# Optimization experiments

Hardware: AMD Instinct MI355X
Metric: run time of the kernel (lower is better)

## Reference

```python
import jax, jax.numpy as jnp
import numpy as np

NUM_HEADS = 12


def _qkv_split(x, qkv_w, num_heads):
    B, N, C = x.shape
    hd = C // num_heads
    qkv = (x @ qkv_w).reshape(B, N, 3, num_heads, hd)
    qkv = jnp.transpose(qkv, (2, 0, 3, 1, 4))  # [3, B, H, N, hd]
    return qkv[0], qkv[1], qkv[2]


def setup_inputs() -> dict:
    key = jax.random.key(0)
    k1, k2, k3, k4 = jax.random.split(key, 4)
    B, N, C = 8, 1024, 768
    s = 0.02
    return {
        "x1": jax.random.normal(k1, (B, N, C), dtype=jnp.float32),
        "x2": jax.random.normal(k2, (B, N, C), dtype=jnp.float32),
        "qkv_w": jax.random.normal(k3, (C, 3 * C), dtype=jnp.float32) * s,
        "proj_w": jax.random.normal(k4, (C, C), dtype=jnp.float32) * s,
        "proj_b": jnp.zeros((C,), dtype=jnp.float32),
    }


def reference(x1, x2, qkv_w, proj_w, proj_b):
    B, N, C = x1.shape
    H = NUM_HEADS
    hd = C // H
    scale = hd ** (-0.5)

    q, k, v = _qkv_split(x1, qkv_w, H)    # each [B, H, N, hd]
    q2, k2, v2 = _qkv_split(x2, qkv_w, H)

    # self-attention branch: q attends to k/v (from x1)
    attn1 = jax.nn.softmax(jnp.einsum('bhqd,bhkd->bhqk', q, k) * scale, axis=-1)
    o1 = jnp.einsum('bhqk,bhkd->bhqd', attn1, v)

    # cross-attention branch: same q attends to k2/v2 (from x2)
    attn2 = jax.nn.softmax(jnp.einsum('bhqd,bhkd->bhqk', q, k2) * scale, axis=-1)
    o2 = jnp.einsum('bhqk,bhkd->bhqd', attn2, v2)

    o1 = jnp.transpose(o1, (0, 2, 1, 3)).reshape(B, N, C) @ proj_w + proj_b
    o2 = jnp.transpose(o2, (0, 2, 1, 3)).reshape(B, N, C) @ proj_w + proj_b
    return (o1, o2)
```

## Files before the change

kernel.cpp:

```cpp
#include <hip/hip_runtime.h>
#include <hip/hip_bf16.h>

#define N_ 1024
#define C_ 768
#define H_ 12

typedef unsigned short u16;
typedef __attribute__((ext_vector_type(8))) short bf16x8;
typedef __attribute__((ext_vector_type(4))) float f32x4;
typedef __attribute__((ext_vector_type(16))) float f32x16;

#define MFMA16(a, b, c) __builtin_amdgcn_mfma_f32_16x16x32_bf16(a, b, c, 0, 0, 0)
#define MFMA32(a, b, c) __builtin_amdgcn_mfma_f32_32x32x16_bf16(a, b, c, 0, 0, 0)

#define GLDS16(gp, lp) __builtin_amdgcn_global_load_lds(                     \
    (const __attribute__((address_space(1))) void*)(gp),                     \
    (__attribute__((address_space(3))) void*)(lp), 16, 0, 0)

__device__ __forceinline__ u16 f2bu(float x) {
    unsigned u = __float_as_uint(x);
    unsigned r = (u + 0x7fffu + ((u >> 16) & 1u)) >> 16;
    return (u16)r;
}

__device__ __forceinline__ unsigned cvtpk(float a, float b) {
    unsigned d;
    asm("v_cvt_pk_bf16_f32 %0, %1, %2" : "=v"(d) : "v"(a), "v"(b));
    return d;
}

__global__ __launch_bounds__(256) void cvt_x(
    const float* __restrict__ x1, const float* __restrict__ x2,
    u16* __restrict__ d1, u16* __restrict__ d2)
{
    const size_t G = 786432;
    for (size_t i = (size_t)blockIdx.x * 256 + threadIdx.x; i < 2 * G;
         i += (size_t)gridDim.x * 256) {
        const float* src = (i < G) ? x1 : x2;
        u16* dst = (i < G) ? d1 : d2;
        size_t g = (i < G) ? i : i - G;
        float4 f0 = ((const float4*)src)[g * 2];
        float4 f1 = ((const float4*)src)[g * 2 + 1];
        ushort4 lo, hi;
        lo.x = f2bu(f0.x); lo.y = f2bu(f0.y); lo.z = f2bu(f0.z); lo.w = f2bu(f0.w);
        hi.x = f2bu(f1.x); hi.y = f2bu(f1.y); hi.z = f2bu(f1.z); hi.w = f2bu(f1.w);
        ((ushort4*)dst)[g * 2] = lo;
        ((ushort4*)dst)[g * 2 + 1] = hi;
    }
}

__global__ __launch_bounds__(256) void tr_cvt(
    const float* __restrict__ W, u16* __restrict__ WT, int R, int CC)
{
    __shared__ float t[32][33];
    const int tx = threadIdx.x & 31, ty = threadIdx.x >> 5;
    const int c0 = blockIdx.x * 32, r0 = blockIdx.y * 32;
#pragma unroll
    for (int i = 0; i < 4; ++i) {
        int r = ty + i * 8;
        t[r][tx] = W[(size_t)(r0 + r) * CC + c0 + tx];
    }
    __syncthreads();
#pragma unroll
    for (int i = 0; i < 4; ++i) {
        int c = ty + i * 8;
        WT[(size_t)(c0 + c) * R + r0 + tx] = f2bu(t[tx][c]);
    }
}

__global__ __launch_bounds__(256) void qkv_gemm(
    const u16* __restrict__ A1, const u16* __restrict__ A2,
    const u16* __restrict__ BT, u16* __restrict__ qd,
    u16* __restrict__ k1d, u16* __restrict__ k2d,
    u16* __restrict__ vt1d, u16* __restrict__ vt2d)
{
    __shared__ u16 As[2][128 * 64];
    __shared__ u16 Bs[2][128 * 64];
    const int tid = threadIdx.x;
    const int w = tid >> 6, lane = tid & 63;
    const int c31 = lane & 31, h = lane >> 5;
    const int wm = w >> 1, wn = w & 1;
    const int id = blockIdx.x;
    const int xcd = id & 7, j = id >> 3;
    const int by = xcd * 8 + j / 30;
    const int bx = j % 30;
    const bool first = bx < 18;
    const u16* A = first ? A1 : A2;
    const int row0 = by * 128;
    const int nc0 = first ? bx * 128 : 768 + (bx - 18) * 128;

    f32x16 acc[2][2];
#pragma unroll
    for (int i = 0; i < 2; ++i)
#pragma unroll
        for (int jj = 0; jj < 2; ++jj)
#pragma unroll
            for (int e = 0; e < 16; ++e) acc[i][jj][e] = 0.f;

    int aoff[4], boff[4];
    {
        const int srow = tid >> 3;
        const int sch = ((tid & 7) ^ (srow & 7)) * 8;
#pragma unroll
        for (int i = 0; i < 4; ++i) {
            int row = i * 32 + srow;
            aoff[i] = (row0 + row) * C_ + sch;
            boff[i] = (nc0 + row) * C_ + sch;
        }
    }
    char* adst0 = (char*)&As[0][0] + w * 1024;
    char* bdst0 = (char*)&Bs[0][0] + w * 1024;
    auto stage = [&](int buf, int k0) {
#pragma unroll
        for (int i = 0; i < 4; ++i) {
            GLDS16(A + aoff[i] + k0, adst0 + buf * 16384 + i * 4096);
            GLDS16(BT + boff[i] + k0, bdst0 + buf * 16384 + i * 4096);
        }
    };

    const int ra0 = wm * 64 + c31, ra1 = ra0 + 32;
    const int rb0 = wn * 64 + c31, rb1 = rb0 + 32;

    stage(0, 0);
    for (int kt = 0; kt < 12; ++kt) {
        const int buf = kt & 1;
        if (kt < 11) {
            stage(buf ^ 1, (kt + 1) * 64);
            asm volatile("s_waitcnt vmcnt(8)" ::: "memory");
        } else {
            asm volatile("s_waitcnt vmcnt(0)" ::: "memory");
        }
        __builtin_amdgcn_s_barrier();
        const char* abase = (const char*)&As[0][0] + buf * 16384;
        const char* bbase = (const char*)&Bs[0][0] + buf * 16384;
#pragma unroll
        for (int kh = 0; kh < 4; ++kh) {
            bf16x8 a0 = *(const bf16x8*)(abase + ra0 * 128 + (((2 * kh + h) ^ (ra0 & 7)) * 16));
            bf16x8 a1 = *(const bf16x8*)(abase + ra1 * 128 + (((2 * kh + h) ^ (ra1 & 7)) * 16));
            bf16x8 b0 = *(const bf16x8*)(bbase + rb0 * 128 + (((2 * kh + h) ^ (rb0 & 7)) * 16));
            bf16x8 b1 = *(const bf16x8*)(bbase + rb1 * 128 + (((2 * kh + h) ^ (rb1 & 7)) * 16));
            acc[0][0] = MFMA32(a0, b0, acc[0][0]);
            acc[0][1] = MFMA32(a0, b1, acc[0][1]);
            acc[1][0] = MFMA32(a1, b0, acc[1][0]);
            acc[1][1] = MFMA32(a1, b1, acc[1][1]);
        }
        asm volatile("" ::: "memory");
        __builtin_amdgcn_s_barrier();
    }

    u16* kd  = first ? k1d : k2d;
    u16* vtd = first ? vt1d : vt2d;
    const int abscol = nc0 + wn * 64;
    const int sec = abscol / C_;
    const int hh = (abscol % C_) >> 6;
    const float scl = (sec == 0) ? 0.180336877f : 1.0f;
#pragma unroll
    for (int mt = 0; mt < 2; ++mt)
#pragma unroll
        for (int nt = 0; nt < 2; ++nt)
#pragma unroll
            for (int r = 0; r < 16; ++r) {
                int row = row0 + wm * 64 + mt * 32 + (r & 3) + 8 * (r >> 2) + 4 * h;
                int b = row >> 10, n = row & 1023;
                int d = nt * 32 + c31;
                u16 val = f2bu(acc[mt][nt][r] * scl);
                size_t bh = (size_t)(b * H_ + hh);
                if (sec == 0)      qd[(bh * N_ + n) * 64 + d] = val;
                else if (sec == 1) kd[(bh * N_ + n) * 64 + d] = val;
                else {
                    int nprm = (n & ~63) | (((n & 15) << 2) | ((n >> 4) & 3));
                    vtd[(bh * 64 + d) * N_ + nprm] = val;
                }
            }
}

__global__ __launch_bounds__(256) void proj_gemm(
    const u16* __restrict__ A1, const u16* __restrict__ A2,
    const u16* __restrict__ BT, const float* __restrict__ bias,
    float* __restrict__ out)
{
    __shared__ u16 As[2][128 * 64];
    __shared__ u16 Bs[2][128 * 64];
    const int tid = threadIdx.x;
    const int w = tid >> 6, lane = tid & 63;
    const int c31 = lane & 31, h = lane >> 5;
    const int wm = w >> 1, wn = w & 1;
    const int sel = blockIdx.y >> 6;
    const u16* A = sel ? A2 : A1;
    float* op = out + (size_t)sel * 8192 * C_;
    const int row0 = (blockIdx.y & 63) * 128;
    const int nc0 = blockIdx.x * 128;

    f32x16 acc[2][2];
#pragma unroll
    for (int i = 0; i < 2; ++i)
#pragma unroll
        for (int jj = 0; jj < 2; ++jj)
#pragma unroll
            for (int e = 0; e < 16; ++e) acc[i][jj][e] = 0.f;

    int aoff[4], boff[4];
    {
        const int srow = tid >> 3;
        const int sch = ((tid & 7) ^ (srow & 7)) * 8;
#pragma unroll
        for (int i = 0; i < 4; ++i) {
            int row = i * 32 + srow;
            aoff[i] = (row0 + row) * C_ + sch;
            boff[i] = (nc0 + row) * C_ + sch;
        }
    }
    char* adst0 = (char*)&As[0][0] + w * 1024;
    char* bdst0 = (char*)&Bs[0][0] + w * 1024;
    auto stage = [&](int buf, int k0) {
#pragma unroll
        for (int i = 0; i < 4; ++i) {
            GLDS16(A + aoff[i] + k0, adst0 + buf * 16384 + i * 4096);
            GLDS16(BT + boff[i] + k0, bdst0 + buf * 16384 + i * 4096);
        }
    };

    const int ra0 = wm * 64 + c31, ra1 = ra0 + 32;
    const int rb0 = wn * 64 + c31, rb1 = rb0 + 32;

    stage(0, 0);
    for (int kt = 0; kt < 12; ++kt) {
        const int buf = kt & 1;
        if (kt < 11) {
            stage(buf ^ 1, (kt + 1) * 64);
            asm volatile("s_waitcnt vmcnt(8)" ::: "memory");
        } else {
            asm volatile("s_waitcnt vmcnt(0)" ::: "memory");
        }
        __builtin_amdgcn_s_barrier();
        const char* abase = (const char*)&As[0][0] + buf * 16384;
        const char* bbase = (const char*)&Bs[0][0] + buf * 16384;
#pragma unroll
        for (int kh = 0; kh < 4; ++kh) {
            bf16x8 a0 = *(const bf16x8*)(abase + ra0 * 128 + (((2 * kh + h) ^ (ra0 & 7)) * 16));
            bf16x8 a1 = *(const bf16x8*)(abase + ra1 * 128 + (((2 * kh + h) ^ (ra1 & 7)) * 16));
            bf16x8 b0 = *(const bf16x8*)(bbase + rb0 * 128 + (((2 * kh + h) ^ (rb0 & 7)) * 16));
            bf16x8 b1 = *(const bf16x8*)(bbase + rb1 * 128 + (((2 * kh + h) ^ (rb1 & 7)) * 16));
            acc[0][0] = MFMA32(a0, b0, acc[0][0]);
            acc[0][1] = MFMA32(a0, b1, acc[0][1]);
            acc[1][0] = MFMA32(a1, b0, acc[1][0]);
            acc[1][1] = MFMA32(a1, b1, acc[1][1]);
        }
        asm volatile("" ::: "memory");
        __builtin_amdgcn_s_barrier();
    }

#pragma unroll
    for (int mt = 0; mt < 2; ++mt)
#pragma unroll
        for (int nt = 0; nt < 2; ++nt)
#pragma unroll
            for (int r = 0; r < 16; ++r) {
                int row = row0 + wm * 64 + mt * 32 + (r & 3) + 8 * (r >> 2) + 4 * h;
                int col = nc0 + wn * 64 + nt * 32 + c31;
                op[(size_t)row * C_ + col] = acc[mt][nt][r] + bias[col];
            }
}

__global__ __launch_bounds__(256) void attn_mfma(
    const u16* __restrict__ Q,
    const u16* __restrict__ K1, const u16* __restrict__ VT1,
    const u16* __restrict__ K2, const u16* __restrict__ VT2,
    u16* __restrict__ O1, u16* __restrict__ O2)
{
    __shared__ u16 Ks[2][64 * 64];
    __shared__ u16 Vs[2][64 * 64];
    __shared__ u16 Ps[4][32 * 72];
    const int tid = threadIdx.x;
    const int w = tid >> 6, lane = tid & 63;
    const int g = lane >> 4, ln = lane & 15;
    const int id = blockIdx.x;
    const int xcd = id & 7, j = id >> 3;
    const int unit = j >> 3;
    const int qb = j & 7;
    const int br = unit >= 12;
    const int bh = xcd * 12 + (br ? unit - 12 : unit);
    const int qw = qb * 128 + w * 32;
    const size_t hb = (size_t)bh * N_ * 64;

    const u16* Kb = (br ? K2 : K1) + hb;
    const u16* Vb = (br ? VT2 : VT1) + hb;
    const u16* Qb = Q + hb;
    u16* O        = br ? O2 : O1;

    bf16x8 qf[2][2];
#pragma unroll
    for (int mt = 0; mt < 2; ++mt)
#pragma unroll
        for (int s = 0; s < 2; ++s)
            qf[mt][s] = *(const bf16x8*)(Qb + (size_t)(qw + mt * 16 + ln) * 64 + s * 32 + g * 8);

    f32x4 o[2][4];
    float lsum[2][4];
#pragma unroll
    for (int mt = 0; mt < 2; ++mt) {
#pragma unroll
        for (int t = 0; t < 4; ++t) o[mt][t] = (f32x4){0.f, 0.f, 0.f, 0.f};
#pragma unroll
        for (int r = 0; r < 4; ++r) lsum[mt][r] = 0.f;
    }

    auto stage = [&](int buf, int key0) {
#pragma unroll
        for (int i = 0; i < 2; ++i) {
            int L = (i * 256 + tid) * 16;
            int row = L >> 7;
            int sw = (((L >> 4) & 7) ^ (row & 7)) * 8;
            GLDS16(Kb + (size_t)(key0 + row) * 64 + sw,
                   (char*)&Ks[buf][0] + i * 4096 + w * 1024);
            GLDS16(Vb + (size_t)row * N_ + key0 + sw,
                   (char*)&Vs[buf][0] + i * 4096 + w * 1024);
        }
    };

    u16* pw = &Ps[w][0];
    const int r7 = ln & 7;

    stage(0, 0);
    __syncthreads();
    for (int kt = 0; kt < 16; ++kt) {
        const int buf = kt & 1;
        if (kt < 15) stage(buf ^ 1, (kt + 1) * 64);
        const char* kbase = (const char*)&Ks[buf][0];
        f32x4 st[2][4];
#pragma unroll
        for (int nt = 0; nt < 4; ++nt) {
            const char* krow = kbase + (nt * 16 + ln) * 128;
            bf16x8 kf0 = *(const bf16x8*)(krow + ((g ^ r7) * 16));
            bf16x8 kf1 = *(const bf16x8*)(krow + (((g + 4) ^ r7) * 16));
#pragma unroll
            for (int mt = 0; mt < 2; ++mt) {
                f32x4 z = (f32x4){0.f, 0.f, 0.f, 0.f};
                z = MFMA16(qf[mt][0], kf0, z);
                z = MFMA16(qf[mt][1], kf1, z);
                st[mt][nt] = z;
            }
        }
#pragma unroll
        for (int mt = 0; mt < 2; ++mt)
#pragma unroll
            for (int r = 0; r < 4; ++r) {
                float p0 = __builtin_amdgcn_exp2f(st[mt][0][r]);
                float p1 = __builtin_amdgcn_exp2f(st[mt][1][r]);
                float p2 = __builtin_amdgcn_exp2f(st[mt][2][r]);
                float p3 = __builtin_amdgcn_exp2f(st[mt][3][r]);
                lsum[mt][r] += (p0 + p1) + (p2 + p3);
                uint2 pk;
                pk.x = cvtpk(p0, p1);
                pk.y = cvtpk(p2, p3);
                int prow = mt * 16 + g * 4 + r;
                *(uint2*)((char*)pw + prow * 144 + ln * 8) = pk;
            }
        const char* vbase = (const char*)&Vs[buf][0];
#pragma unroll
        for (int s = 0; s < 2; ++s) {
            bf16x8 pa[2];
            pa[0] = *(const bf16x8*)((const char*)pw + (0 + ln) * 144 + s * 64 + g * 16);
            pa[1] = *(const bf16x8*)((const char*)pw + (16 + ln) * 144 + s * 64 + g * 16);
#pragma unroll
            for (int t = 0; t < 4; ++t) {
                bf16x8 vf = *(const bf16x8*)(vbase + (t * 16 + ln) * 128 + (((s * 4 + g) ^ r7) * 16));
#pragma unroll
                for (int mt = 0; mt < 2; ++mt) o[mt][t] = MFMA16(pa[mt], vf, o[mt][t]);
            }
        }
        __syncthreads();
    }
    const int b = bh / H_, h = bh % H_;
#pragma unroll
    for (int mt = 0; mt < 2; ++mt)
#pragma unroll
        for (int r = 0; r < 4; ++r) {
            float ls = lsum[mt][r];
#pragma unroll
            for (int off = 8; off; off >>= 1) ls += __shfl_xor(ls, off);
            float inv = 1.f / ls;
            int n = qw + mt * 16 + g * 4 + r;
            u16* orow = O + ((size_t)(b * N_) + n) * C_ + h * 64 + ln;
#pragma unroll
            for (int t = 0; t < 4; ++t)
                orow[t * 16] = f2bu(o[mt][t][r] * inv);
        }
}

extern "C" void kernel_launch(void* const* d_in, const int* in_sizes, int n_in,
                              void* d_out, int out_size, void* d_ws, size_t ws_size,
                              hipStream_t stream) {
    const float* x1     = (const float*)d_in[0];
    const float* x2     = (const float*)d_in[1];
    const float* qkv_w  = (const float*)d_in[2];
    const float* proj_w = (const float*)d_in[3];
    const float* proj_b = (const float*)d_in[4];
    float* out = (float*)d_out;

    u16* ws = (u16*)d_ws;
    const size_t SZ = (size_t)8 * H_ * N_ * 64;
    u16* wqkvT  = ws;
    u16* wprojT = wqkvT + (size_t)2304 * 768;
    u16* q      = wprojT + (size_t)768 * 768;
    u16* k1     = q + SZ;
    u16* vT1    = k1 + SZ;
    u16* slotA  = vT1 + SZ;
    u16* vT2    = slotA + SZ;
    u16* slotB  = vT2 + SZ;
    u16* x1c = slotA, *o2p = slotA;
    u16* x2c = slotB, *o1p = slotB;
    u16* k2buf = (u16*)(out + SZ);

    cvt_x<<<2048, 256, 0, stream>>>(x1, x2, x1c, x2c);
    tr_cvt<<<dim3(72, 24), 256, 0, stream>>>(qkv_w, wqkvT, C_, 3 * C_);
    tr_cvt<<<dim3(24, 24), 256, 0, stream>>>(proj_w, wprojT, C_, C_);
    qkv_gemm<<<1920, 256, 0, stream>>>(x1c, x2c, wqkvT, q, k1, k2buf, vT1, vT2);
    attn_mfma<<<1536, 256, 0, stream>>>(q, k1, vT1, k2buf, vT2, o1p, o2p);
    proj_gemm<<<dim3(6, 128), 256, 0, stream>>>(o1p, o2p, wprojT, proj_b, out);
}
```

Before: 217.1 us.

## Use 8-wave blocks for QKV and projection GEMMs and remap proj grid per XCD

Both GEMM kernels move from 4 to 8 wavefronts per 128x128 tile. Each wave now computes a 64x32 sub-tile with two accumulators instead of four, and each thread issues half as many global-to-LDS loads per stage. The projection GEMM also switches to a 1D grid with an XCD-aware block mapping so neighbouring row tiles share a chiplet's L2. The aim is more latency hiding and better cache locality, at the cost of less MFMA work per wave and more A-fragment LDS reads per flop.

```diff
diff --git a/kernel.cpp b/kernel.cpp
--- a/kernel.cpp
+++ b/kernel.cpp
@@ -68,7 +68,7 @@
     }
 }
 
-__global__ __launch_bounds__(256) void qkv_gemm(
+__global__ __launch_bounds__(512) void qkv_gemm(
     const u16* __restrict__ A1, const u16* __restrict__ A2,
     const u16* __restrict__ BT, u16* __restrict__ qd,
     u16* __restrict__ k1d, u16* __restrict__ k2d,
@@ -79,7 +79,7 @@
     const int tid = threadIdx.x;
     const int w = tid >> 6, lane = tid & 63;
     const int c31 = lane & 31, h = lane >> 5;
-    const int wm = w >> 1, wn = w & 1;
+    const int wm = w >> 2, wn = w & 3;
     const int id = blockIdx.x;
     const int xcd = id & 7, j = id >> 3;
     const int by = xcd * 8 + j / 30;
@@ -89,44 +89,40 @@
     const int row0 = by * 128;
     const int nc0 = first ? bx * 128 : 768 + (bx - 18) * 128;
 
-    f32x16 acc[2][2];
+    f32x16 acc[2];
 #pragma unroll
     for (int i = 0; i < 2; ++i)
 #pragma unroll
-        for (int jj = 0; jj < 2; ++jj)
-#pragma unroll
-            for (int e = 0; e < 16; ++e) acc[i][jj][e] = 0.f;
-
-    int aoff[4], boff[4];
-    {
-        const int srow = tid >> 3;
-        const int sch = ((tid & 7) ^ (srow & 7)) * 8;
-#pragma unroll
-        for (int i = 0; i < 4; ++i) {
-            int row = i * 32 + srow;
-            aoff[i] = (row0 + row) * C_ + sch;
-            boff[i] = (nc0 + row) * C_ + sch;
-        }
+        for (int e = 0; e < 16; ++e) acc[i][e] = 0.f;
+
+    const int srow = tid >> 3;
+    const int sch = ((tid & 7) ^ (srow & 7)) * 8;
+    int aoff[2], boff[2];
+#pragma unroll
+    for (int i = 0; i < 2; ++i) {
+        int row = i * 64 + srow;
+        aoff[i] = (row0 + row) * C_ + sch;
+        boff[i] = (nc0 + row) * C_ + sch;
     }
     char* adst0 = (char*)&As[0][0] + w * 1024;
     char* bdst0 = (char*)&Bs[0][0] + w * 1024;
     auto stage = [&](int buf, int k0) {
 #pragma unroll
-        for (int i = 0; i < 4; ++i) {
-            GLDS16(A + aoff[i] + k0, adst0 + buf * 16384 + i * 4096);
-            GLDS16(BT + boff[i] + k0, bdst0 + buf * 16384 + i * 4096);
+        for (int i = 0; i < 2; ++i) {
+            GLDS16(A + aoff[i] + k0, adst0 + buf * 16384 + i * 8192);
+            GLDS16(BT + boff[i] + k0, bdst0 + buf * 16384 + i * 8192);
         }
     };
 
     const int ra0 = wm * 64 + c31, ra1 = ra0 + 32;
-    const int rb0 = wn * 64 + c31, rb1 = rb0 + 32;
+    const int rb0 = wn * 32 + c31;
 
     stage(0, 0);
     for (int kt = 0; kt < 12; ++kt) {
         const int buf = kt & 1;
         if (kt < 11) {
             stage(buf ^ 1, (kt + 1) * 64);
-            asm volatile("s_waitcnt vmcnt(8)" ::: "memory");
+            asm volatile("s_waitcnt vmcnt(4)" ::: "memory");
         } else {
             asm volatile("s_waitcnt vmcnt(0)" ::: "memory");
         }
@@ -138,11 +134,8 @@
             bf16x8 a0 = *(const bf16x8*)(abase + ra0 * 128 + (((2 * kh + h) ^ (ra0 & 7)) * 16));
             bf16x8 a1 = *(const bf16x8*)(abase + ra1 * 128 + (((2 * kh + h) ^ (ra1 & 7)) * 16));
             bf16x8 b0 = *(const bf16x8*)(bbase + rb0 * 128 + (((2 * kh + h) ^ (rb0 & 7)) * 16));
-            bf16x8 b1 = *(const bf16x8*)(bbase + rb1 * 128 + (((2 * kh + h) ^ (rb1 & 7)) * 16));
-            acc[0][0] = MFMA32(a0, b0, acc[0][0]);
-            acc[0][1] = MFMA32(a0, b1, acc[0][1]);
-            acc[1][0] = MFMA32(a1, b0, acc[1][0]);
-            acc[1][1] = MFMA32(a1, b1, acc[1][1]);
+            acc[0] = MFMA32(a0, b0, acc[0]);
+            acc[1] = MFMA32(a1, b0, acc[1]);
         }
         asm volatile("" ::: "memory");
         __builtin_amdgcn_s_barrier();
@@ -150,31 +143,29 @@
 
     u16* kd  = first ? k1d : k2d;
     u16* vtd = first ? vt1d : vt2d;
-    const int abscol = nc0 + wn * 64;
-    const int sec = abscol / C_;
-    const int hh = (abscol % C_) >> 6;
+    const int col = nc0 + wn * 32 + c31;
+    const int sec = col / C_;
+    const int hh = (col % C_) >> 6;
+    const int d = col & 63;
     const float scl = (sec == 0) ? 0.180336877f : 1.0f;
 #pragma unroll
     for (int mt = 0; mt < 2; ++mt)
 #pragma unroll
-        for (int nt = 0; nt < 2; ++nt)
-#pragma unroll
-            for (int r = 0; r < 16; ++r) {
-                int row = row0 + wm * 64 + mt * 32 + (r & 3) + 8 * (r >> 2) + 4 * h;
-                int b = row >> 10, n = row & 1023;
-                int d = nt * 32 + c31;
-                u16 val = f2bu(acc[mt][nt][r] * scl);
-                size_t bh = (size_t)(b * H_ + hh);
-                if (sec == 0)      qd[(bh * N_ + n) * 64 + d] = val;
-                else if (sec == 1) kd[(bh * N_ + n) * 64 + d] = val;
-                else {
-                    int nprm = (n & ~63) | (((n & 15) << 2) | ((n >> 4) & 3));
-                    vtd[(bh * 64 + d) * N_ + nprm] = val;
-                }
+        for (int r = 0; r < 16; ++r) {
+            int row = row0 + wm * 64 + mt * 32 + (r & 3) + 8 * (r >> 2) + 4 * h;
+            int b = row >> 10, n = row & 1023;
+            u16 val = f2bu(acc[mt][r] * scl);
+            size_t bh = (size_t)(b * H_ + hh);
+            if (sec == 0)      qd[(bh * N_ + n) * 64 + d] = val;
+            else if (sec == 1) kd[(bh * N_ + n) * 64 + d] = val;
+            else {
+                int nprm = (n & ~63) | (((n & 15) << 2) | ((n >> 4) & 3));
+                vtd[(bh * 64 + d) * N_ + nprm] = val;
             }
-}
-
-__global__ __launch_bounds__(256) void proj_gemm(
+        }
+}
+
+__global__ __launch_bounds__(512) void proj_gemm(
     const u16* __restrict__ A1, const u16* __restrict__ A2,
     const u16* __restrict__ BT, const float* __restrict__ bias,
     float* __restrict__ out)
@@ -184,51 +175,50 @@
     const int tid = threadIdx.x;
     const int w = tid >> 6, lane = tid & 63;
     const int c31 = lane & 31, h = lane >> 5;
-    const int wm = w >> 1, wn = w & 1;
-    const int sel = blockIdx.y >> 6;
+    const int wm = w >> 2, wn = w & 3;
+    const int id = blockIdx.x;
+    const int xcd = id & 7, j = id >> 3;
+    const int byg = xcd * 16 + j / 6;
+    const int sel = byg >> 6;
     const u16* A = sel ? A2 : A1;
     float* op = out + (size_t)sel * 8192 * C_;
-    const int row0 = (blockIdx.y & 63) * 128;
-    const int nc0 = blockIdx.x * 128;
-
-    f32x16 acc[2][2];
+    const int row0 = (byg & 63) * 128;
+    const int nc0 = (j % 6) * 128;
+
+    f32x16 acc[2];
 #pragma unroll
     for (int i = 0; i < 2; ++i)
 #pragma unroll
-        for (int jj = 0; jj < 2; ++jj)
-#pragma unroll
-            for (int e = 0; e < 16; ++e) acc[i][jj][e] = 0.f;
-
-    int aoff[4], boff[4];
-    {
-        const int srow = tid >> 3;
-        const int sch = ((tid & 7) ^ (srow & 7)) * 8;
-#pragma unroll
-        for (int i = 0; i < 4; ++i) {
-            int row = i * 32 + srow;
-            aoff[i] = (row0 + row) * C_ + sch;
-            boff[i] = (nc0 + row) * C_ + sch;
-        }
+        for (int e = 0; e < 16; ++e) acc[i][e] = 0.f;
+
+    const int srow = tid >> 3;
+    const int sch = ((tid & 7) ^ (srow & 7)) * 8;
+    int aoff[2], boff[2];
+#pragma unroll
+    for (int i = 0; i < 2; ++i) {
+        int row = i * 64 + srow;
+        aoff[i] = (row0 + row) * C_ + sch;
+        boff[i] = (nc0 + row) * C_ + sch;
     }
     char* adst0 = (char*)&As[0][0] + w * 1024;
     char* bdst0 = (char*)&Bs[0][0] + w * 1024;
     auto stage = [&](int buf, int k0) {
 #pragma unroll
-        for (int i = 0; i < 4; ++i) {
-            GLDS16(A + aoff[i] + k0, adst0 + buf * 16384 + i * 4096);
-            GLDS16(BT + boff[i] + k0, bdst0 + buf * 16384 + i * 4096);
+        for (int i = 0; i < 2; ++i) {
+            GLDS16(A + aoff[i] + k0, adst0 + buf * 16384 + i * 8192);
+            GLDS16(BT + boff[i] + k0, bdst0 + buf * 16384 + i * 8192);
         }
     };
 
     const int ra0 = wm * 64 + c31, ra1 = ra0 + 32;
-    const int rb0 = wn * 64 + c31, rb1 = rb0 + 32;
+    const int rb0 = wn * 32 + c31;
 
     stage(0, 0);
     for (int kt = 0; kt < 12; ++kt) {
         const int buf = kt & 1;
         if (kt < 11) {
             stage(buf ^ 1, (kt + 1) * 64);
-            asm volatile("s_waitcnt vmcnt(8)" ::: "memory");
+            asm volatile("s_waitcnt vmcnt(4)" ::: "memory");
         } else {
             asm volatile("s_waitcnt vmcnt(0)" ::: "memory");
         }
@@ -240,26 +230,21 @@
             bf16x8 a0 = *(const bf16x8*)(abase + ra0 * 128 + (((2 * kh + h) ^ (ra0 & 7)) * 16));
             bf16x8 a1 = *(const bf16x8*)(abase + ra1 * 128 + (((2 * kh + h) ^ (ra1 & 7)) * 16));
             bf16x8 b0 = *(const bf16x8*)(bbase + rb0 * 128 + (((2 * kh + h) ^ (rb0 & 7)) * 16));
-            bf16x8 b1 = *(const bf16x8*)(bbase + rb1 * 128 + (((2 * kh + h) ^ (rb1 & 7)) * 16));
-            acc[0][0] = MFMA32(a0, b0, acc[0][0]);
-            acc[0][1] = MFMA32(a0, b1, acc[0][1]);
-            acc[1][0] = MFMA32(a1, b0, acc[1][0]);
-            acc[1][1] = MFMA32(a1, b1, acc[1][1]);
+            acc[0] = MFMA32(a0, b0, acc[0]);
+            acc[1] = MFMA32(a1, b0, acc[1]);
         }
         asm volatile("" ::: "memory");
         __builtin_amdgcn_s_barrier();
     }
 
+    const int col = nc0 + wn * 32 + c31;
 #pragma unroll
     for (int mt = 0; mt < 2; ++mt)
 #pragma unroll
-        for (int nt = 0; nt < 2; ++nt)
-#pragma unroll
-            for (int r = 0; r < 16; ++r) {
-                int row = row0 + wm * 64 + mt * 32 + (r & 3) + 8 * (r >> 2) + 4 * h;
-                int col = nc0 + wn * 64 + nt * 32 + c31;
-                op[(size_t)row * C_ + col] = acc[mt][nt][r] + bias[col];
-            }
+        for (int r = 0; r < 16; ++r) {
+            int row = row0 + wm * 64 + mt * 32 + (r & 3) + 8 * (r >> 2) + 4 * h;
+            op[(size_t)row * C_ + col] = acc[mt][r] + bias[col];
+        }
 }
 
 __global__ __launch_bounds__(256) void attn_mfma(
@@ -415,7 +400,7 @@
     cvt_x<<<2048, 256, 0, stream>>>(x1, x2, x1c, x2c);
     tr_cvt<<<dim3(72, 24), 256, 0, stream>>>(qkv_w, wqkvT, C_, 3 * C_);
     tr_cvt<<<dim3(24, 24), 256, 0, stream>>>(proj_w, wprojT, C_, C_);
-    qkv_gemm<<<1920, 256, 0, stream>>>(x1c, x2c, wqkvT, q, k1, k2buf, vT1, vT2);
+    qkv_gemm<<<1920, 512, 0, stream>>>(x1c, x2c, wqkvT, q, k1, k2buf, vT1, vT2);
     attn_mfma<<<1536, 256, 0, stream>>>(q, k1, vT1, k2buf, vT2, o1p, o2p);
-    proj_gemm<<<dim3(6, 128), 256, 0, stream>>>(o1p, o2p, wprojT, proj_b, out);
-}
+    proj_gemm<<<768, 512, 0, stream>>>(o1p, o2p, wprojT, proj_b, out);
+}
```

New measurement: 206.4 us, median of 2. 4.9% less time.
